# Performance work log

Hardware: AMD Instinct MI355X
Metric: run time of the kernel (lower is better)

The kernel has to match this reference:

```python
import jax, jax.numpy as jnp
import numpy as np

H, HKV, DH = 32, 8, 128
ROPE_BASE = 500000.0


def _rope(x, pos):
    # x: [B, H, T, D]; MLX non-traditional rope (split halves)
    D = x.shape[-1]
    half = D // 2
    freqs = ROPE_BASE ** (-(jnp.arange(half, dtype=jnp.float32) * 2.0 / D))  # [half]
    t = pos + jnp.arange(x.shape[2], dtype=jnp.float32)                      # [T]
    ang = t[:, None] * freqs[None, :]                                        # [T, half]
    cos, sin = jnp.cos(ang), jnp.sin(ang)
    x1, x2 = x[..., :half], x[..., half:]
    return jnp.concatenate([x1 * cos - x2 * sin, x1 * sin + x2 * cos], axis=-1)


def setup_inputs() -> dict:
    key = jax.random.key(0)
    ks = jax.random.split(key, 5)
    B, T, HID = 1, 2048, 4096
    s = 0.02
    return {
        "hidden_states": jax.random.normal(ks[0], (B, T, HID), jnp.float32),
        "Wq": jax.random.normal(ks[1], (H * DH, HID), jnp.float32) * s,
        "Wk": jax.random.normal(ks[2], (HKV * DH, HID), jnp.float32) * s,
        "Wv": jax.random.normal(ks[3], (HKV * DH, HID), jnp.float32) * s,
        "Wo": jax.random.normal(ks[4], (HID, H * DH), jnp.float32) * s,
        "k_cache": jnp.zeros((1, HKV, 4096, DH), jnp.float32),
        "v_cache": jnp.zeros((1, HKV, 4096, DH), jnp.float32),
        "pos_int": 0,
    }


def reference(hidden_states, Wq, Wk, Wv, Wo, k_cache, v_cache, pos_int):
    B, T, _ = hidden_states.shape
    # QKV projections (no bias, Llama-style) -> [B, h, T, D]
    q = (hidden_states @ Wq.T).reshape(B, T, H, DH).transpose(0, 2, 1, 3)
    k = (hidden_states @ Wk.T).reshape(B, T, HKV, DH).transpose(0, 2, 1, 3)
    v = (hidden_states @ Wv.T).reshape(B, T, HKV, DH).transpose(0, 2, 1, 3)
    # RoPE with position offset
    q = _rope(q, pos_int)
    k = _rope(k, pos_int)
    # KV-cache scatter update at pos_int, then window to [:pos_int+T]
    k_cache = jax.lax.dynamic_update_slice(k_cache, k, (0, 0, pos_int, 0))
    v_cache = jax.lax.dynamic_update_slice(v_cache, v, (0, 0, pos_int, 0))
    Tk = pos_int + T
    k_win = k_cache[:, :, :Tk, :]
    v_win = v_cache[:, :, :Tk, :]
    # GQA: repeat_interleave KV heads to match query heads
    group = H // HKV
    k_ = jnp.repeat(k_win, group, axis=1)   # [B, H, Tk, D]
    v_ = jnp.repeat(v_win, group, axis=1)
    # SDPA, is_causal=True => top-left aligned causal mask (query i sees keys j<=i)
    scale = 1.0 / jnp.sqrt(jnp.asarray(DH, jnp.float32))
    scores = jnp.einsum("bhtd,bhsd->bhts", q, k_) * scale  # [B, H, T, Tk]
    causal = jnp.arange(Tk)[None, :] <= jnp.arange(T)[:, None]
    scores = jnp.where(causal[None, None], scores, jnp.finfo(scores.dtype).min)
    attn = jax.nn.softmax(scores, axis=-1)
    out = jnp.einsum("bhts,bhsd->bhtd", attn, v_)           # [B, H, T, D]
    out = out.transpose(0, 2, 1, 3).reshape(B, T, H * DH)
    return out @ Wo.T
```

## Files before the change

kernel.cpp:

```cpp
#include <hip/hip_runtime.h>


#define DEVI __device__ __forceinline__

typedef __attribute__((ext_vector_type(8))) short short8;
typedef __attribute__((ext_vector_type(4))) float f32x4;

DEVI unsigned short f2bf(float f) {
  union { float f; unsigned u; } x; x.f = f;
  unsigned r = x.u + 0x7FFFu + ((x.u >> 16) & 1u);
  return (unsigned short)(r >> 16);
}
DEVI float bf2f(unsigned short h) {
  union { unsigned u; float f; } x; x.u = ((unsigned)h) << 16;
  return x.f;
}
DEVI f32x4 mfma16(short8 a, short8 b, f32x4 c) {
  return __builtin_amdgcn_mfma_f32_16x16x32_bf16(a, b, c, 0, 0, 0);
}
DEVI void gl2lds16(const unsigned short* g, unsigned short* l) {
  __builtin_amdgcn_global_load_lds(
      (const __attribute__((address_space(1))) unsigned int*)g,
      (__attribute__((address_space(3))) unsigned int*)l, 16, 0, 0);
}
DEVI void bar() { __builtin_amdgcn_s_barrier(); }
DEVI void sfence() { __builtin_amdgcn_sched_barrier(0); }

DEVI void cvt_region(const float* __restrict__ src,
                     unsigned short* __restrict__ dst, int n4, int start,
                     int stride) {
  for (int i = start; i < n4; i += stride) {
    float4 v = ((const float4*)src)[i];
    ushort4 h;
    h.x = f2bf(v.x); h.y = f2bf(v.y); h.z = f2bf(v.z); h.w = f2bf(v.w);
    ((ushort4*)dst)[i] = h;
  }
}
__global__ __launch_bounds__(256)
void cvt5_kernel(const float* __restrict__ s0, const float* __restrict__ s1,
                 const float* __restrict__ s2, const float* __restrict__ s3,
                 const float* __restrict__ s4,
                 unsigned short* __restrict__ d0, unsigned short* __restrict__ d1,
                 unsigned short* __restrict__ d2, unsigned short* __restrict__ d3,
                 unsigned short* __restrict__ d4,
                 int n0, int n1, int n2, int n3, int n4) {
  const int start = blockIdx.x * 256 + threadIdx.x;
  const int stride = gridDim.x * 256;
  cvt_region(s0, d0, n0, start, stride);
  cvt_region(s1, d1, n1, start, stride);
  cvt_region(s2, d2, n2, start, stride);
  cvt_region(s3, d3, n3, start, stride);
  cvt_region(s4, d4, n4, start, stride);
}

__global__ __launch_bounds__(512, 2)
void gemm_qkv_8ph(const unsigned short* __restrict__ hsb,
                  const unsigned short* __restrict__ Wqb,
                  const unsigned short* __restrict__ Wkb,
                  const unsigned short* __restrict__ Wvb,
                  unsigned short* __restrict__ Qb,
                  unsigned short* __restrict__ Kb,
                  unsigned short* __restrict__ Vb) {
  const int K = 4096;
  const int NT = 64;
  __shared__ __align__(16) unsigned short Ls[2][2][2][256][32];
  const int tid = threadIdx.x, lane = tid & 63, w = tid >> 6;
  const int wr = w >> 2, wc = w & 3;
  const int bid = blockIdx.x;
  const int m0 = (bid & 7) * 256;
  const int n0g = (bid >> 3) * 256;

  const unsigned short* Bsrc; unsigned short* outp; int ldo, oc;
  if (n0g < 4096)      { Bsrc = Wqb + (size_t)n0g * K;          outp = Qb; ldo = 4096; oc = n0g; }
  else if (n0g < 5120) { Bsrc = Wkb + (size_t)(n0g - 4096) * K; outp = Kb; ldo = 1024; oc = n0g - 4096; }
  else                 { Bsrc = Wvb + (size_t)(n0g - 5120) * K; outp = Vb; ldo = 1024; oc = n0g - 5120; }
  const unsigned short* Asrc = hsb + (size_t)m0 * K;

  auto stageU = [&](const unsigned short* src, int ab, int kh, int tt, int bb) {
#pragma unroll
    for (int j = 0; j < 2; ++j) {
      const int seg = j * 8 + w;
      const int row = seg * 16 + (lane >> 2);
      const int cs  = (lane & 3) ^ ((row >> 1) & 3);
      gl2lds16(src + (size_t)row * K + tt * 64 + kh * 32 + cs * 8,
               &Ls[bb][ab][kh][seg * 16][0]);
    }
  };
  auto ldA = [&](int bb, int kh, int fm) -> short8 {
    const int ra = wr * 128 + fm * 16 + (lane & 15);
    const int cs = (lane >> 4) ^ ((ra >> 1) & 3);
    return *(const short8*)&Ls[bb][0][kh][ra][cs * 8];
  };
  auto ldB = [&](int bb, int kh, int fn) -> short8 {
    const int rb = wc * 64 + fn * 16 + (lane & 15);
    const int cs = (lane >> 4) ^ ((rb >> 1) & 3);
    return *(const short8*)&Ls[bb][1][kh][rb][cs * 8];
  };

  f32x4 acc[8][4];
#pragma unroll
  for (int i = 0; i < 8; ++i)
#pragma unroll
    for (int j = 0; j < 4; ++j) acc[i][j] = (f32x4){0.f, 0.f, 0.f, 0.f};

  stageU(Asrc, 0, 0, 0, 0);
  stageU(Asrc, 0, 1, 0, 0);
  stageU(Bsrc, 1, 0, 0, 0);
  stageU(Bsrc, 1, 1, 0, 0);
  stageU(Bsrc, 1, 0, 1, 1);
  stageU(Asrc, 0, 0, 1, 1);
  stageU(Bsrc, 1, 1, 1, 1);
  asm volatile("s_waitcnt vmcnt(6)" ::: "memory");
  bar();
  sfence();

  short8 af[4], bfr[4];
  for (int t = 0; t < NT; ++t) {
    const int bb = t & 1, nb = bb ^ 1;
#pragma unroll
    for (int i = 0; i < 4; ++i) af[i] = ldA(bb, 0, i);
#pragma unroll
    for (int i = 0; i < 4; ++i) bfr[i] = ldB(bb, 0, i);
    if (t + 1 < NT) stageU(Asrc, 0, 1, t + 1, nb);
    bar();
    __builtin_amdgcn_s_setprio(1);
#pragma unroll
    for (int i = 0; i < 4; ++i)
#pragma unroll
      for (int j = 0; j < 4; ++j) acc[i][j] = mfma16(af[i], bfr[j], acc[i][j]);
    __builtin_amdgcn_s_setprio(0);
    sfence(); bar(); sfence();
#pragma unroll
    for (int i = 0; i < 4; ++i) af[i] = ldA(bb, 0, 4 + i);
    if (t + 2 < NT) stageU(Bsrc, 1, 0, t + 2, bb);
    bar();
    __builtin_amdgcn_s_setprio(1);
#pragma unroll
    for (int i = 0; i < 4; ++i)
#pragma unroll
      for (int j = 0; j < 4; ++j) acc[4 + i][j] = mfma16(af[i], bfr[j], acc[4 + i][j]);
    __builtin_amdgcn_s_setprio(0);
    sfence(); bar(); sfence();
#pragma unroll
    for (int i = 0; i < 4; ++i) af[i] = ldA(bb, 1, i);
#pragma unroll
    for (int i = 0; i < 4; ++i) bfr[i] = ldB(bb, 1, i);
    if (t + 2 < NT) stageU(Asrc, 0, 0, t + 2, bb);
    bar();
    __builtin_amdgcn_s_setprio(1);
#pragma unroll
    for (int i = 0; i < 4; ++i)
#pragma unroll
      for (int j = 0; j < 4; ++j) acc[i][j] = mfma16(af[i], bfr[j], acc[i][j]);
    __builtin_amdgcn_s_setprio(0);
    sfence(); bar(); sfence();
#pragma unroll
    for (int i = 0; i < 4; ++i) af[i] = ldA(bb, 1, 4 + i);
    if (t + 2 < NT) stageU(Bsrc, 1, 1, t + 2, bb);
    bar();
    __builtin_amdgcn_s_setprio(1);
#pragma unroll
    for (int i = 0; i < 4; ++i)
#pragma unroll
      for (int j = 0; j < 4; ++j) acc[4 + i][j] = mfma16(af[i], bfr[j], acc[4 + i][j]);
    __builtin_amdgcn_s_setprio(0);
    if (t < NT - 2) asm volatile("s_waitcnt vmcnt(6)" ::: "memory");
    else            asm volatile("s_waitcnt vmcnt(0)" ::: "memory");
    sfence(); bar(); sfence();
  }

#pragma unroll
  for (int fm = 0; fm < 8; ++fm) {
    const int rb0 = m0 + wr * 128 + fm * 16 + ((lane >> 4) << 2);
#pragma unroll
    for (int fn = 0; fn < 4; ++fn) {
      const int cb = oc + wc * 64 + fn * 16 + (lane & 15);
#pragma unroll
      for (int r = 0; r < 4; ++r)
        outp[(size_t)(rb0 + r) * ldo + cb] = f2bf(acc[fm][fn][r]);
    }
  }
}

__global__ __launch_bounds__(256)
void postproc_kernel(const unsigned short* __restrict__ Vb,
                     unsigned short* __restrict__ VtG,
                     unsigned short* __restrict__ Qb,
                     unsigned short* __restrict__ Kb,
                     const int* __restrict__ posp) {
  __shared__ unsigned short tile[64][68];
  const int b = blockIdx.x, tid = threadIdx.x;
  if (b < 512) {
    const int t0 = (b & 31) * 64;
    const int c0 = (b >> 5) * 64;
    const int r = tid >> 4;
    const int c4 = (tid & 15) << 2;
#pragma unroll
    for (int i = 0; i < 4; ++i) {
      ushort4 v = *(const ushort4*)(Vb + (size_t)(t0 + r + i * 16) * 1024 + c0 + c4);
      *(ushort4*)&tile[r + i * 16][c4] = v;
    }
    __syncthreads();
#pragma unroll
    for (int i = 0; i < 4; ++i) {
      int d = r + i * 16;
      ushort4 o;
      o.x = tile[c4 + 0][d]; o.y = tile[c4 + 1][d];
      o.z = tile[c4 + 2][d]; o.w = tile[c4 + 3][d];
      *(ushort4*)(VtG + (size_t)(c0 + d) * 2048 + t0 + c4) = o;
    }
    return;
  }
  const int QP = 2048 * 32 * 64;
  const int KP = 2048 * 8 * 64;
  int idx = (b - 512) * 256 + tid;
  if (idx >= QP + KP) return;
  unsigned short* base; int t, hh, d, ld;
  if (idx < QP) {
    base = Qb; ld = 4096;
    t = idx >> 11; int rem = idx & 2047; hh = rem >> 6; d = rem & 63;
  } else {
    int j = idx - QP; base = Kb; ld = 1024;
    t = j >> 9; int rem = j & 511; hh = rem >> 6; d = rem & 63;
  }
  float freq = exp2f(-(float)d * 0.29580575880077f);
  float ang = (float)(t + posp[0]) * freq;
  float s, c;
  __sincosf(ang, &s, &c);
  size_t i1 = (size_t)t * ld + hh * 128 + d;
  float x1 = bf2f(base[i1]), x2 = bf2f(base[i1 + 64]);
  base[i1]      = f2bf(x1 * c - x2 * s);
  base[i1 + 64] = f2bf(x1 * s + x2 * c);
}

__global__ __launch_bounds__(512)
void attn_kernel(const unsigned short* __restrict__ Qb,
                 const unsigned short* __restrict__ Kb,
                 const unsigned short* __restrict__ VtG,
                 unsigned short* __restrict__ Ob) {
  __shared__ __align__(16) unsigned short Ks[2][64][128];
  __shared__ __align__(16) unsigned short Vt[2][128][64];
  __shared__ __align__(16) unsigned short Ps[8][16][64];
  const int tid = threadIdx.x, lane = tid & 63, w = tid >> 6;
  const int b = blockIdx.x;
  const int kh = b & 7;
  const int h  = kh * 4 + ((b >> 3) & 3);
  const int qi = b >> 5;
  const int qt = (qi < 8) ? qi : 23 - qi;
  const int q0 = qt * 128;
  const float SCALE = 0.08838834764831845f;

  short8 aq[4];
  {
    const int qrow = q0 + w * 16 + (lane & 15);
#pragma unroll
    for (int ks = 0; ks < 4; ++ks)
      aq[ks] = *(const short8*)(Qb + (size_t)qrow * 4096 + h * 128 + ks * 32 +
                                ((lane >> 4) << 3));
  }

  f32x4 o_acc[8];
#pragma unroll
  for (int n8 = 0; n8 < 8; ++n8) o_acc[n8] = (f32x4){0.f, 0.f, 0.f, 0.f};
  float mst[4], lst[4];
#pragma unroll
  for (int r = 0; r < 4; ++r) { mst[r] = -1e30f; lst[r] = 0.f; }

  auto stage = [&](int st, int bb) {
    const int s0 = st * 64;
#pragma unroll
    for (int j = 0; j < 2; ++j) {
      int sr = w * 8 + j * 4 + (lane >> 4);
      int sc = (((lane & 15) << 4) ^ ((sr & 7) << 4)) >> 1;
      gl2lds16(Kb + (size_t)(s0 + sr) * 1024 + kh * 128 + sc,
               &Ks[bb][w * 8 + j * 4][0]);
    }
#pragma unroll
    for (int j = 0; j < 2; ++j) {
      int dr = w * 16 + j * 8 + (lane >> 3);
      int sc = (((lane & 7) << 4) ^ ((dr & 7) << 4)) >> 1;
      gl2lds16(VtG + (size_t)(kh * 128 + dr) * 2048 + s0 + sc,
               &Vt[bb][w * 16 + j * 8][0]);
    }
  };

  const int ntiles = 2 * (qt + 1);
  stage(0, 0);
  for (int st = 0; st < ntiles; ++st) {
    const int cb = st & 1;
    const int s0 = st * 64;
    if (st + 1 < ntiles) {
      stage(st + 1, cb ^ 1);
      asm volatile("s_waitcnt vmcnt(4)" ::: "memory");
    } else {
      asm volatile("s_waitcnt vmcnt(0)" ::: "memory");
    }
    bar(); sfence();

    f32x4 sacc[4];
#pragma unroll
    for (int ni = 0; ni < 4; ++ni) sacc[ni] = (f32x4){0.f, 0.f, 0.f, 0.f};
#pragma unroll
    for (int ks = 0; ks < 4; ++ks) {
      const int co = ks * 64 + ((lane >> 4) << 4);
      short8 bk[4];
#pragma unroll
      for (int ni = 0; ni < 4; ++ni) {
        int kr = ni * 16 + (lane & 15);
        bk[ni] = *(const short8*)((const char*)(&Ks[cb][kr][0]) + (co ^ ((kr & 7) << 4)));
      }
#pragma unroll
      for (int ni = 0; ni < 4; ++ni)
        sacc[ni] = mfma16(aq[ks], bk[ni], sacc[ni]);
    }

    char* pb = (char*)(&Ps[w][0][0]);
#pragma unroll
    for (int r = 0; r < 4; ++r) {
      const int qrow = q0 + w * 16 + ((lane >> 4) << 2) + r;
      float v4[4]; float vmax = -1e30f;
#pragma unroll
      for (int ni = 0; ni < 4; ++ni) {
        int scol = s0 + ni * 16 + (lane & 15);
        float x = sacc[ni][r] * SCALE;
        if (scol > qrow) x = -1e30f;
        v4[ni] = x; vmax = fmaxf(vmax, x);
      }
      vmax = fmaxf(vmax, __shfl_xor(vmax, 1));
      vmax = fmaxf(vmax, __shfl_xor(vmax, 2));
      vmax = fmaxf(vmax, __shfl_xor(vmax, 4));
      vmax = fmaxf(vmax, __shfl_xor(vmax, 8));
      float mo = mst[r];
      float mn = fmaxf(mo, vmax);
      float al = __expf(mo - mn);
      float rs = 0.f;
      const int prow = ((lane >> 4) << 2) + r;
      const int pswz = ((prow >> 2) & 3) << 5;
#pragma unroll
      for (int ni = 0; ni < 4; ++ni) {
        float p = __expf(v4[ni] - mn);
        rs += p;
        int cbyte = (ni * 16 + (lane & 15)) * 2;
        *(unsigned short*)(pb + prow * 128 + (cbyte ^ pswz)) = f2bf(p);
      }
      rs += __shfl_xor(rs, 1);
      rs += __shfl_xor(rs, 2);
      rs += __shfl_xor(rs, 4);
      rs += __shfl_xor(rs, 8);
      lst[r] = lst[r] * al + rs;
      mst[r] = mn;
#pragma unroll
      for (int n8 = 0; n8 < 8; ++n8) o_acc[n8][r] *= al;
    }

#pragma unroll
    for (int ks2 = 0; ks2 < 2; ++ks2) {
      const int co = ks2 * 64 + ((lane >> 4) << 4);
      const int pr = lane & 15;
      short8 pa = *(const short8*)(pb + pr * 128 + (co ^ (((pr >> 2) & 3) << 5)));
#pragma unroll
      for (int n8 = 0; n8 < 8; ++n8) {
        int vr = n8 * 16 + (lane & 15);
        short8 bv = *(const short8*)((const char*)(&Vt[cb][vr][0]) + (co ^ ((vr & 7) << 4)));
        o_acc[n8] = mfma16(pa, bv, o_acc[n8]);
      }
    }
    sfence(); bar(); sfence();
  }

#pragma unroll
  for (int r = 0; r < 4; ++r) {
    float inv = 1.0f / lst[r];
    int row = q0 + w * 16 + ((lane >> 4) << 2) + r;
#pragma unroll
    for (int n8 = 0; n8 < 8; ++n8)
      Ob[(size_t)row * 4096 + h * 128 + n8 * 16 + (lane & 15)] =
          f2bf(o_acc[n8][r] * inv);
  }
}

__global__ __launch_bounds__(256, 2)
void gemm_out_bf16(const unsigned short* __restrict__ Ab,
                   const unsigned short* __restrict__ Wob,
                   float* __restrict__ Cout) {
  const int K = 4096;
  __shared__ __align__(16) unsigned short As[128][64];
  __shared__ __align__(16) unsigned short Bs[128][64];
  const int tid = threadIdx.x, lane = tid & 63, wid = tid >> 6;
  const int bid = blockIdx.x;
  const int m0 = (((bid & 7) + 8 * (bid >> 8))) * 128;
  const int n0 = ((bid >> 3) & 31) * 128;
  const unsigned short* Asrc = Ab + (size_t)m0 * K;
  const unsigned short* Bsrc = Wob + (size_t)n0 * K;

  f32x4 acc[4][4];
#pragma unroll
  for (int i = 0; i < 4; ++i)
#pragma unroll
    for (int j = 0; j < 4; ++j) acc[i][j] = (f32x4){0.f, 0.f, 0.f, 0.f};

  const int wm = (wid >> 1) * 64, wn = (wid & 1) * 64;
  const int srow = wid * 32 + (lane >> 3);
  const int scol = (lane & 7) * 8;

  for (int k0 = 0; k0 < K; k0 += 64) {
#pragma unroll
    for (int i = 0; i < 4; ++i) {
      gl2lds16(Asrc + (size_t)(srow + i * 8) * K + k0 + scol, &As[wid * 32 + i * 8][0]);
      gl2lds16(Bsrc + (size_t)(srow + i * 8) * K + k0 + scol, &Bs[wid * 32 + i * 8][0]);
    }
    __syncthreads();
#pragma unroll
    for (int ks = 0; ks < 2; ++ks) {
      short8 af[4], bfr[4];
      const int co = ks * 64 + ((lane >> 4) << 4);
#pragma unroll
      for (int i = 0; i < 4; ++i) {
        af[i]  = *(const short8*)((const char*)(&As[wm + i * 16 + (lane & 15)][0]) + co);
        bfr[i] = *(const short8*)((const char*)(&Bs[wn + i * 16 + (lane & 15)][0]) + co);
      }
#pragma unroll
      for (int i = 0; i < 4; ++i)
#pragma unroll
        for (int j = 0; j < 4; ++j)
          acc[i][j] = mfma16(af[i], bfr[j], acc[i][j]);
    }
    __syncthreads();
  }

#pragma unroll
  for (int i = 0; i < 4; ++i) {
    int rb = m0 + wm + i * 16 + ((lane >> 4) << 2);
#pragma unroll
    for (int j = 0; j < 4; ++j) {
      int cb = n0 + wn + j * 16 + (lane & 15);
#pragma unroll
      for (int r = 0; r < 4; ++r)
        Cout[(size_t)(rb + r) * 4096 + cb] = acc[i][j][r];
    }
  }
}

extern "C" void kernel_launch(void* const* d_in, const int* in_sizes, int n_in,
                              void* d_out, int out_size, void* d_ws, size_t ws_size,
                              hipStream_t stream) {
  const float* hs = (const float*)d_in[0];
  const float* Wq = (const float*)d_in[1];
  const float* Wk = (const float*)d_in[2];
  const float* Wv = (const float*)d_in[3];
  const float* Wo = (const float*)d_in[4];
  const int* pos = (const int*)d_in[7];

  unsigned short* hsb = (unsigned short*)d_ws;
  unsigned short* Wqb = hsb + (size_t)8  * 1024 * 1024;
  unsigned short* Wkb = Wqb + (size_t)16 * 1024 * 1024;
  unsigned short* Wvb = Wkb + (size_t)4  * 1024 * 1024;
  unsigned short* Wob = Wvb + (size_t)4  * 1024 * 1024;
  unsigned short* Qb  = Wob + (size_t)16 * 1024 * 1024;
  unsigned short* Kb  = Qb  + (size_t)8  * 1024 * 1024;
  unsigned short* Vb  = Kb  + (size_t)2  * 1024 * 1024;
  unsigned short* Ob  = Vb  + (size_t)2  * 1024 * 1024;
  unsigned short* VtG = hsb;
  float* out = (float*)d_out;

  cvt5_kernel<<<dim3(2048), 256, 0, stream>>>(
      hs, Wq, Wk, Wv, Wo, hsb, Wqb, Wkb, Wvb, Wob,
      2 * 1024 * 1024, 4 * 1024 * 1024, 1 * 1024 * 1024, 1 * 1024 * 1024,
      4 * 1024 * 1024);

  gemm_qkv_8ph<<<dim3(192), 512, 0, stream>>>(hsb, Wqb, Wkb, Wvb, Qb, Kb, Vb);

  const int npairs = 2048 * 32 * 64 + 2048 * 8 * 64;
  const int rope_blocks = (npairs + 255) / 256;
  postproc_kernel<<<dim3(512 + rope_blocks), 256, 0, stream>>>(Vb, VtG, Qb, Kb, pos);

  attn_kernel<<<dim3(512), 512, 0, stream>>>(Qb, Kb, VtG, Ob);
  gemm_out_bf16<<<dim3(512), 256, 0, stream>>>(Ob, Wob, out);
}
```

Measured before the change: 359.7 us.

## Retile QKV GEMM to 128x192 blocks and add lazy softmax rescaling

The fused QKV projection moves from 192 blocks of 256x256 tiles (512 threads) to 512 blocks of 128x192 tiles (256 threads). It treats Wq, Wk and Wv as one contiguous weight matrix and picks the Q/K/V output buffer per 16-column fragment, so the grid fills more CUs on the 256-CU part. The attention kernel also skips the online-softmax max update and accumulator rescale unless some lane's new max exceeds the running max by more than 8. This saves exp and multiply work, and it relies on bounded exp growth (up to e^8) for fp32 and bf16 accuracy.

```diff
diff --git a/kernel.cpp b/kernel.cpp
--- a/kernel.cpp
+++ b/kernel.cpp
@@ -53,128 +53,129 @@
   cvt_region(s4, d4, n4, start, stride);
 }
 
-__global__ __launch_bounds__(512, 2)
-void gemm_qkv_8ph(const unsigned short* __restrict__ hsb,
-                  const unsigned short* __restrict__ Wqb,
-                  const unsigned short* __restrict__ Wkb,
-                  const unsigned short* __restrict__ Wvb,
-                  unsigned short* __restrict__ Qb,
-                  unsigned short* __restrict__ Kb,
-                  unsigned short* __restrict__ Vb) {
-  const int K = 4096;
-  const int NT = 64;
-  __shared__ __align__(16) unsigned short Ls[2][2][2][256][32];
+__global__ __launch_bounds__(256, 2)
+void gemm_qkv_12(const unsigned short* __restrict__ hsb,
+                 const unsigned short* __restrict__ Wall,
+                 unsigned short* __restrict__ Qb,
+                 unsigned short* __restrict__ Kb,
+                 unsigned short* __restrict__ Vb) {
+  const int K = 4096, NT = 64;
+  __shared__ __align__(16) unsigned short LA[2][2][128][32];
+  __shared__ __align__(16) unsigned short LB[2][2][192][32];
   const int tid = threadIdx.x, lane = tid & 63, w = tid >> 6;
-  const int wr = w >> 2, wc = w & 3;
+  const int wr = w >> 1, wc = w & 1;
   const int bid = blockIdx.x;
-  const int m0 = (bid & 7) * 256;
-  const int n0g = (bid >> 3) * 256;
-
-  const unsigned short* Bsrc; unsigned short* outp; int ldo, oc;
-  if (n0g < 4096)      { Bsrc = Wqb + (size_t)n0g * K;          outp = Qb; ldo = 4096; oc = n0g; }
-  else if (n0g < 5120) { Bsrc = Wkb + (size_t)(n0g - 4096) * K; outp = Kb; ldo = 1024; oc = n0g - 4096; }
-  else                 { Bsrc = Wvb + (size_t)(n0g - 5120) * K; outp = Vb; ldo = 1024; oc = n0g - 5120; }
+  const int m0 = (bid >> 5) * 128;
+  const int n0g = (bid & 31) * 192;
   const unsigned short* Asrc = hsb + (size_t)m0 * K;
-
-  auto stageU = [&](const unsigned short* src, int ab, int kh, int tt, int bb) {
+  const unsigned short* Bsrc = Wall + (size_t)n0g * K;
+
+  auto stageA = [&](int kh, int tt, int bb) {
 #pragma unroll
     for (int j = 0; j < 2; ++j) {
-      const int seg = j * 8 + w;
-      const int row = seg * 16 + (lane >> 2);
-      const int cs  = (lane & 3) ^ ((row >> 1) & 3);
-      gl2lds16(src + (size_t)row * K + tt * 64 + kh * 32 + cs * 8,
-               &Ls[bb][ab][kh][seg * 16][0]);
+      const int row = j * 64 + (tid >> 2);
+      const int cs = (tid & 3) ^ ((row >> 1) & 3);
+      gl2lds16(Asrc + (size_t)row * K + tt * 64 + kh * 32 + cs * 8,
+               &LA[bb][kh][j * 64 + w * 16][0]);
+    }
+  };
+  auto stageB = [&](int kh, int tt, int bb) {
+#pragma unroll
+    for (int j = 0; j < 3; ++j) {
+      const int row = j * 64 + (tid >> 2);
+      const int cs = (tid & 3) ^ ((row >> 1) & 3);
+      gl2lds16(Bsrc + (size_t)row * K + tt * 64 + kh * 32 + cs * 8,
+               &LB[bb][kh][j * 64 + w * 16][0]);
     }
   };
   auto ldA = [&](int bb, int kh, int fm) -> short8 {
-    const int ra = wr * 128 + fm * 16 + (lane & 15);
+    const int ra = wr * 64 + fm * 16 + (lane & 15);
     const int cs = (lane >> 4) ^ ((ra >> 1) & 3);
-    return *(const short8*)&Ls[bb][0][kh][ra][cs * 8];
+    return *(const short8*)&LA[bb][kh][ra][cs * 8];
   };
   auto ldB = [&](int bb, int kh, int fn) -> short8 {
-    const int rb = wc * 64 + fn * 16 + (lane & 15);
+    const int rb = wc * 96 + fn * 16 + (lane & 15);
     const int cs = (lane >> 4) ^ ((rb >> 1) & 3);
-    return *(const short8*)&Ls[bb][1][kh][rb][cs * 8];
+    return *(const short8*)&LB[bb][kh][rb][cs * 8];
   };
 
-  f32x4 acc[8][4];
-#pragma unroll
-  for (int i = 0; i < 8; ++i)
-#pragma unroll
-    for (int j = 0; j < 4; ++j) acc[i][j] = (f32x4){0.f, 0.f, 0.f, 0.f};
-
-  stageU(Asrc, 0, 0, 0, 0);
-  stageU(Asrc, 0, 1, 0, 0);
-  stageU(Bsrc, 1, 0, 0, 0);
-  stageU(Bsrc, 1, 1, 0, 0);
-  stageU(Bsrc, 1, 0, 1, 1);
-  stageU(Asrc, 0, 0, 1, 1);
-  stageU(Bsrc, 1, 1, 1, 1);
-  asm volatile("s_waitcnt vmcnt(6)" ::: "memory");
-  bar();
-  sfence();
-
-  short8 af[4], bfr[4];
+  f32x4 acc[4][6];
+#pragma unroll
+  for (int i = 0; i < 4; ++i)
+#pragma unroll
+    for (int j = 0; j < 6; ++j) acc[i][j] = (f32x4){0.f, 0.f, 0.f, 0.f};
+
+  stageA(0, 0, 0); stageA(1, 0, 0); stageB(0, 0, 0); stageB(1, 0, 0);
+  stageB(0, 1, 1); stageA(0, 1, 1); stageB(1, 1, 1);
+  asm volatile("s_waitcnt vmcnt(8)" ::: "memory");
+  bar(); sfence();
+
+  short8 af[2], bfr[6];
   for (int t = 0; t < NT; ++t) {
     const int bb = t & 1, nb = bb ^ 1;
 #pragma unroll
-    for (int i = 0; i < 4; ++i) af[i] = ldA(bb, 0, i);
-#pragma unroll
-    for (int i = 0; i < 4; ++i) bfr[i] = ldB(bb, 0, i);
-    if (t + 1 < NT) stageU(Asrc, 0, 1, t + 1, nb);
+    for (int i = 0; i < 2; ++i) af[i] = ldA(bb, 0, i);
+#pragma unroll
+    for (int i = 0; i < 6; ++i) bfr[i] = ldB(bb, 0, i);
+    if (t + 1 < NT) stageA(1, t + 1, nb);
     bar();
     __builtin_amdgcn_s_setprio(1);
 #pragma unroll
-    for (int i = 0; i < 4; ++i)
-#pragma unroll
-      for (int j = 0; j < 4; ++j) acc[i][j] = mfma16(af[i], bfr[j], acc[i][j]);
+    for (int i = 0; i < 2; ++i)
+#pragma unroll
+      for (int j = 0; j < 6; ++j) acc[i][j] = mfma16(af[i], bfr[j], acc[i][j]);
     __builtin_amdgcn_s_setprio(0);
     sfence(); bar(); sfence();
 #pragma unroll
-    for (int i = 0; i < 4; ++i) af[i] = ldA(bb, 0, 4 + i);
-    if (t + 2 < NT) stageU(Bsrc, 1, 0, t + 2, bb);
+    for (int i = 0; i < 2; ++i) af[i] = ldA(bb, 0, 2 + i);
+    if (t + 2 < NT) stageB(0, t + 2, bb);
     bar();
     __builtin_amdgcn_s_setprio(1);
 #pragma unroll
-    for (int i = 0; i < 4; ++i)
-#pragma unroll
-      for (int j = 0; j < 4; ++j) acc[4 + i][j] = mfma16(af[i], bfr[j], acc[4 + i][j]);
+    for (int i = 0; i < 2; ++i)
+#pragma unroll
+      for (int j = 0; j < 6; ++j) acc[2 + i][j] = mfma16(af[i], bfr[j], acc[2 + i][j]);
     __builtin_amdgcn_s_setprio(0);
     sfence(); bar(); sfence();
 #pragma unroll
-    for (int i = 0; i < 4; ++i) af[i] = ldA(bb, 1, i);
-#pragma unroll
-    for (int i = 0; i < 4; ++i) bfr[i] = ldB(bb, 1, i);
-    if (t + 2 < NT) stageU(Asrc, 0, 0, t + 2, bb);
+    for (int i = 0; i < 2; ++i) af[i] = ldA(bb, 1, i);
+#pragma unroll
+    for (int i = 0; i < 6; ++i) bfr[i] = ldB(bb, 1, i);
+    if (t + 2 < NT) stageA(0, t + 2, bb);
     bar();
     __builtin_amdgcn_s_setprio(1);
 #pragma unroll
-    for (int i = 0; i < 4; ++i)
-#pragma unroll
-      for (int j = 0; j < 4; ++j) acc[i][j] = mfma16(af[i], bfr[j], acc[i][j]);
+    for (int i = 0; i < 2; ++i)
+#pragma unroll
+      for (int j = 0; j < 6; ++j) acc[i][j] = mfma16(af[i], bfr[j], acc[i][j]);
     __builtin_amdgcn_s_setprio(0);
     sfence(); bar(); sfence();
 #pragma unroll
-    for (int i = 0; i < 4; ++i) af[i] = ldA(bb, 1, 4 + i);
-    if (t + 2 < NT) stageU(Bsrc, 1, 1, t + 2, bb);
+    for (int i = 0; i < 2; ++i) af[i] = ldA(bb, 1, 2 + i);
+    if (t + 2 < NT) stageB(1, t + 2, bb);
     bar();
     __builtin_amdgcn_s_setprio(1);
 #pragma unroll
-    for (int i = 0; i < 4; ++i)
-#pragma unroll
-      for (int j = 0; j < 4; ++j) acc[4 + i][j] = mfma16(af[i], bfr[j], acc[4 + i][j]);
+    for (int i = 0; i < 2; ++i)
+#pragma unroll
+      for (int j = 0; j < 6; ++j) acc[2 + i][j] = mfma16(af[i], bfr[j], acc[2 + i][j]);
     __builtin_amdgcn_s_setprio(0);
-    if (t < NT - 2) asm volatile("s_waitcnt vmcnt(6)" ::: "memory");
+    if (t < NT - 2) asm volatile("s_waitcnt vmcnt(8)" ::: "memory");
     else            asm volatile("s_waitcnt vmcnt(0)" ::: "memory");
     sfence(); bar(); sfence();
   }
 
 #pragma unroll
-  for (int fm = 0; fm < 8; ++fm) {
-    const int rb0 = m0 + wr * 128 + fm * 16 + ((lane >> 4) << 2);
-#pragma unroll
-    for (int fn = 0; fn < 4; ++fn) {
-      const int cb = oc + wc * 64 + fn * 16 + (lane & 15);
+  for (int fm = 0; fm < 4; ++fm) {
+    const int rb0 = m0 + wr * 64 + fm * 16 + ((lane >> 4) << 2);
+#pragma unroll
+    for (int fn = 0; fn < 6; ++fn) {
+      const int cbase = n0g + wc * 96 + fn * 16;
+      unsigned short* outp; int ldo, oc;
+      if (cbase < 4096)      { outp = Qb; ldo = 4096; oc = cbase; }
+      else if (cbase < 5120) { outp = Kb; ldo = 1024; oc = cbase - 4096; }
+      else                   { outp = Vb; ldo = 1024; oc = cbase - 5120; }
+      const int cb = oc + (lane & 15);
 #pragma unroll
       for (int r = 0; r < 4; ++r)
         outp[(size_t)(rb0 + r) * ldo + cb] = f2bf(acc[fm][fn][r]);
@@ -331,14 +332,21 @@
       vmax = fmaxf(vmax, __shfl_xor(vmax, 4));
       vmax = fmaxf(vmax, __shfl_xor(vmax, 8));
       float mo = mst[r];
-      float mn = fmaxf(mo, vmax);
-      float al = __expf(mo - mn);
+      if (!__all(vmax <= mo + 8.0f)) {
+        float mn = fmaxf(mo, vmax);
+        float al = __expf(mo - mn);
+        lst[r] *= al;
+#pragma unroll
+        for (int n8 = 0; n8 < 8; ++n8) o_acc[n8][r] *= al;
+        mst[r] = mn;
+      }
+      float m_use = mst[r];
       float rs = 0.f;
       const int prow = ((lane >> 4) << 2) + r;
       const int pswz = ((prow >> 2) & 3) << 5;
 #pragma unroll
       for (int ni = 0; ni < 4; ++ni) {
-        float p = __expf(v4[ni] - mn);
+        float p = __expf(v4[ni] - m_use);
         rs += p;
         int cbyte = (ni * 16 + (lane & 15)) * 2;
         *(unsigned short*)(pb + prow * 128 + (cbyte ^ pswz)) = f2bf(p);
@@ -347,10 +355,7 @@
       rs += __shfl_xor(rs, 2);
       rs += __shfl_xor(rs, 4);
       rs += __shfl_xor(rs, 8);
-      lst[r] = lst[r] * al + rs;
-      mst[r] = mn;
-#pragma unroll
-      for (int n8 = 0; n8 < 8; ++n8) o_acc[n8][r] *= al;
+      lst[r] += rs;
     }
 
 #pragma unroll
@@ -468,7 +473,7 @@
       2 * 1024 * 1024, 4 * 1024 * 1024, 1 * 1024 * 1024, 1 * 1024 * 1024,
       4 * 1024 * 1024);
 
-  gemm_qkv_8ph<<<dim3(192), 512, 0, stream>>>(hsb, Wqb, Wkb, Wvb, Qb, Kb, Vb);
+  gemm_qkv_12<<<dim3(512), 256, 0, stream>>>(hsb, Wqb, Qb, Kb, Vb);
 
   const int npairs = 2048 * 32 * 64 + 2048 * 8 * 64;
   const int rope_blocks = (npairs + 255) / 256;
```

After: 362.5 us. About the same (+0.8%).
